# Performance work log

Hardware: AMD Instinct MI355X
Metric: run time of the kernel (lower is better)

Reference implementation:

```python
import jax, jax.numpy as jnp
import numpy as np

HID = 32      # STGAT hidden_dim
HEADS = 8
NHID = HID // HEADS  # per-head hidden = 4
NEG_SLOPE = 0.2


def lstm_layer(x, Wih, Whh, bih, bhh):
    # x: (BN, T, H_in); torch gate order i, f, g, o
    BN = x.shape[0]
    H = Whh.shape[1]
    b = bih + bhh

    def step(carry, xt):
        h, c = carry
        z = xt @ Wih.T + h @ Whh.T + b
        i, f, g, o = jnp.split(z, 4, axis=-1)
        c = jax.nn.sigmoid(f) * c + jax.nn.sigmoid(i) * jnp.tanh(g)
        h = jax.nn.sigmoid(o) * jnp.tanh(c)
        return (h, c), h

    h0 = jnp.zeros((BN, H), x.dtype)
    _, ys = jax.lax.scan(step, (h0, h0), jnp.swapaxes(x, 0, 1))
    return jnp.swapaxes(ys, 0, 1)  # (BN, T, H)


def setup_inputs():
    key = jax.random.key(0)
    ks = jax.random.split(key, 16)
    B, N, T_in, F_in = 8, 300, 12, 3
    T_out, F_out = 12, 3
    X = jax.random.normal(ks[0], (B, N, T_in, F_in), jnp.float32)
    adj = (jax.random.uniform(ks[1], (N, N)) < 0.05).astype(jnp.float32)
    A_hat = jnp.maximum(adj, jnp.eye(N, dtype=jnp.float32))  # self-loops

    def init(k, shape, fan):
        return jax.random.normal(k, shape, jnp.float32) / np.float32(np.sqrt(fan))

    W_gat = init(ks[2], (HID, F_in), F_in)          # linear (no bias)
    a_attn = init(ks[3], (2 * NHID,), 2 * NHID)     # attn (no bias), flattened (1, 2*nhid)
    W_ih0 = init(ks[4], (4 * HID, HID), HID)
    W_hh0 = init(ks[5], (4 * HID, HID), HID)
    b_ih0 = init(ks[6], (4 * HID,), HID)
    b_hh0 = init(ks[7], (4 * HID,), HID)
    W_ih1 = init(ks[8], (4 * HID, HID), HID)
    W_hh1 = init(ks[9], (4 * HID, HID), HID)
    b_ih1 = init(ks[10], (4 * HID,), HID)
    b_hh1 = init(ks[11], (4 * HID,), HID)
    fc_W = init(ks[12], (F_out * T_out, HID), HID)
    fc_b = init(ks[13], (F_out * T_out,), HID)
    return {"A_hat": A_hat, "X": X, "W_gat": W_gat, "a_attn": a_attn,
            "W_ih0": W_ih0, "W_hh0": W_hh0, "b_ih0": b_ih0, "b_hh0": b_hh0,
            "W_ih1": W_ih1, "W_hh1": W_hh1, "b_ih1": b_ih1, "b_hh1": b_hh1,
            "fc_W": fc_W, "fc_b": fc_b}


def reference(A_hat, X, W_gat, a_attn, W_ih0, W_hh0, b_ih0, b_hh0,
              W_ih1, W_hh1, b_ih1, b_hh1, fc_W, fc_b):
    B, N, T, F = X.shape
    T_out = fc_W.shape[0] // F  # nums_feature_output == F here

    # --- GAT, vectorized over (batch, timestep) ---
    # g: (B, N, T, HEADS, NHID)
    g = (X @ W_gat.T).reshape(B, N, T, HEADS, NHID)
    a_l, a_r = a_attn[:NHID], a_attn[NHID:]
    # attn(g_concat) = a_l . g_i + a_r . g_j  (exact split of the concat+linear)
    gl = jnp.einsum('bithd,d->bith', g, a_l)
    gr = jnp.einsum('bjthd,d->bjth', g, a_r)
    e = jax.nn.leaky_relu(gl[:, :, None] + gr[:, None, :], NEG_SLOPE)  # (B,i,j,T,H)
    mask = (A_hat == 0)[None, :, :, None, None]
    e = jnp.where(mask, -jnp.inf, e)
    a = jax.nn.softmax(e, axis=2)  # softmax over j (dim=1 of the (i,j,h) tensor)
    h_gat = jnp.einsum('bijth,bjthd->bithd', a, g).reshape(B, N, T, HID)

    # --- 2-layer LSTM over time, per (b, n) sequence ---
    lstm_in = h_gat.reshape(B * N, T, HID)
    h1 = lstm_layer(lstm_in, W_ih0, W_hh0, b_ih0, b_hh0)
    h2 = lstm_layer(h1, W_ih1, W_hh1, b_ih1, b_hh1)
    h_last = h2[:, -1, :]  # (B*N, HID)

    out = h_last @ fc_W.T + fc_b
    return out.reshape(B, N, T_out, F)
```

## Files before the change

### kernel.cpp

```cpp
#include <hip/hip_runtime.h>

typedef __attribute__((ext_vector_type(8))) short s8v;
typedef __attribute__((ext_vector_type(4))) float f4v;

__device__ __forceinline__ float sgm(float x) { return 1.f / (1.f + __expf(-x)); }
__device__ __forceinline__ float tanh_fast(float x) {
    float e = __expf(-2.f * fabsf(x));
    float t = (1.f - e) / (1.f + e);
    return copysignf(t, x);
}
__device__ __forceinline__ void bsplit(float x, short& hi, short& lo) {
    unsigned u = __float_as_uint(x);
    unsigned hb = u & 0xffff0000u;
    hi = (short)(hb >> 16);
    float r = x - __uint_as_float(hb);
    lo = (short)(__float_as_uint(r) >> 16);
}

#define SQ 10

__device__ __forceinline__ void zcomp(const short* vh, const short* vl,
    const s8v (&ah)[2], const s8v (&al)[2], f4v bias, float* zdst,
    int boff, int g, int w, int n16)
{
    s8v bh0 = *(const s8v*)((const char*)vh + boff +      g*16);
    s8v bh1 = *(const s8v*)((const char*)vh + boff + 64 + g*16);
    s8v bl0 = *(const s8v*)((const char*)vl + boff +      g*16);
    s8v bl1 = *(const s8v*)((const char*)vl + boff + 64 + g*16);
    f4v acc = bias;
    acc = __builtin_amdgcn_mfma_f32_16x16x32_bf16(ah[0], bh0, acc, 0, 0, 0);
    acc = __builtin_amdgcn_mfma_f32_16x16x32_bf16(ah[1], bh1, acc, 0, 0, 0);
    acc = __builtin_amdgcn_mfma_f32_16x16x32_bf16(al[0], bh0, acc, 0, 0, 0);
    acc = __builtin_amdgcn_mfma_f32_16x16x32_bf16(al[1], bh1, acc, 0, 0, 0);
    acc = __builtin_amdgcn_mfma_f32_16x16x32_bf16(ah[0], bl0, acc, 0, 0, 0);
    acc = __builtin_amdgcn_mfma_f32_16x16x32_bf16(ah[1], bl1, acc, 0, 0, 0);
    *(f4v*)&zdst[n16*132 + w*16 + g*4] = acc;
}

__device__ __forceinline__ float cellupd(const float* zbp, int us, int uc, float& cst)
{
    float zi = zbp[us*132 + uc],      zf = zbp[us*132 + 32 + uc];
    float zg = zbp[us*132 + 64 + uc], zo = zbp[us*132 + 96 + uc];
    cst = sgm(zf)*cst + sgm(zi)*tanh_fast(zg);
    return sgm(zo)*tanh_fast(cst);
}

__global__ __launch_bounds__(512, 1) void k_stgat(
    const float* __restrict__ A,    const float* __restrict__ X,
    const float* __restrict__ Wg,   const float* __restrict__ aat,
    const float* __restrict__ Wih0, const float* __restrict__ Whh0,
    const float* __restrict__ bih0, const float* __restrict__ bhh0,
    const float* __restrict__ Wih1, const float* __restrict__ Whh1,
    const float* __restrict__ bih1, const float* __restrict__ bhh1,
    const float* __restrict__ fcW,  const float* __restrict__ fcb,
    float* __restrict__ out)
{
    __shared__ int   snbr[SQ][64];
    __shared__ int   scnt[SQ];
    __shared__ float shg[SQ*384];
    __shared__ __align__(16) short vh0[16*72], vl0[16*72];
    __shared__ __align__(16) short vh1[16*72], vl1[16*72];
    __shared__ __align__(16) float zb0[16*132], zb1[16*132];
    __shared__ float sh1f[SQ*32];

    const int tid  = threadIdx.x;
    const int w    = tid >> 6;
    const int l    = tid & 63;
    const int seq0 = blockIdx.x * SQ;

    for (int r = w; r < SQ; r += 8) {
        int i = (seq0 + r) % 300;
        int c = 0;
        for (int j0 = 0; j0 < 300; j0 += 64) {
            int j = j0 + l;
            bool p = (j < 300) && (A[i*300 + j] != 0.f);
            unsigned long long m = __ballot(p);
            if (p) {
                int pos = __popcll(m & ((1ull << l) - 1ull));
                if (c + pos < 64) snbr[r][c + pos] = j;
            }
            c += __popcll(m);
        }
        if (c > 64) c = 64;
        if (l == 0) scnt[r] = c;
    }

    const int n16  = l & 15;
    const int g    = l >> 4;
    const int zrow = w*16 + n16;
    s8v a0h[2], a0l[2], a1h[2], a1l[2];
    {
        const float* s00 = Wih0 + zrow*32 + g*8;
        const float* s01 = Whh0 + zrow*32 + g*8;
        const float* s10 = Wih1 + zrow*32 + g*8;
        const float* s11 = Whh1 + zrow*32 + g*8;
        #pragma unroll
        for (int j = 0; j < 8; j++) {
            short hh, ll;
            bsplit(s00[j], hh, ll); a0h[0][j]=hh; a0l[0][j]=ll;
            bsplit(s01[j], hh, ll); a0h[1][j]=hh; a0l[1][j]=ll;
            bsplit(s10[j], hh, ll); a1h[0][j]=hh; a1l[0][j]=ll;
            bsplit(s11[j], hh, ll); a1h[1][j]=hh; a1l[1][j]=ll;
        }
    }
    f4v bias0, bias1;
    #pragma unroll
    for (int r = 0; r < 4; r++) {
        int rr = w*16 + g*4 + r;
        bias0[r] = bih0[rr] + bhh0[rr];
        bias1[r] = bih1[rr] + bhh1[rr];
    }

    __syncthreads();

    {
        const int h = l >> 3, j8 = l & 7, d = j8 & 3;
        float wal0=0.f, wal1=0.f, wal2=0.f, war0=0.f, war1=0.f, war2=0.f;
        #pragma unroll
        for (int dd = 0; dd < 4; dd++) {
            float av = aat[dd], bv = aat[4+dd];
            const float* wr = Wg + (h*4+dd)*3;
            wal0 += wr[0]*av; wal1 += wr[1]*av; wal2 += wr[2]*av;
            war0 += wr[0]*bv; war1 += wr[1]*bv; war2 += wr[2]*bv;
        }
        const float* wp = Wg + (h*4+d)*3;
        float wp0 = wp[0], wp1 = wp[1], wp2 = wp[2];

        for (int q = 0; q < 15; q++) {
            int u  = w*15 + q;
            int us = u / 12, t = u - us*12;
            int seq = seq0 + us;
            int b = seq / 300, i = seq - b*300;
            int c = scnt[us];

            const float* Xb = X + (size_t)b*300*36 + t*3;
            const float* Xi = Xb + i*36;
            float gl = Xi[0]*wal0 + Xi[1]*wal1 + Xi[2]*wal2;

            float m = -1e30f, s = 0.f, a0 = 0.f, a1 = 0.f, a2 = 0.f;
            for (int kk = j8; kk < c; kk += 8) {
                int j = snbr[us][kk];
                const float* Xj = Xb + j*36;
                float y0 = Xj[0], y1 = Xj[1], y2 = Xj[2];
                float e = gl + y0*war0 + y1*war1 + y2*war2;
                e = e > 0.f ? e : 0.2f*e;
                if (e > m) {
                    float sc = __expf(m - e);
                    s = s*sc + 1.f;
                    a0 = a0*sc + y0; a1 = a1*sc + y1; a2 = a2*sc + y2;
                    m = e;
                } else {
                    float wt = __expf(e - m);
                    s += wt;
                    a0 += wt*y0; a1 += wt*y1; a2 += wt*y2;
                }
            }
            #pragma unroll
            for (int off = 1; off <= 4; off <<= 1) {
                float m2 = __shfl_xor(m, off, 64);
                float s2 = __shfl_xor(s, off, 64);
                float b0 = __shfl_xor(a0, off, 64);
                float b1 = __shfl_xor(a1, off, 64);
                float b2 = __shfl_xor(a2, off, 64);
                float mo = fmaxf(m, m2);
                float w1 = __expf(m - mo), w2 = __expf(m2 - mo);
                s = s*w1 + s2*w2;
                a0 = a0*w1 + b0*w2; a1 = a1*w1 + b1*w2; a2 = a2*w1 + b2*w2;
                m = mo;
            }
            if (j8 < 4)
                shg[us*384 + t*32 + h*4 + d] = (a0*wp0 + a1*wp1 + a2*wp2) / s;
        }
    }
    __syncthreads();

    const int us = tid >> 5, uc = tid & 31;
    const bool upd = tid < SQ*32;
    const int boff = n16 * 144;

    if (upd) {
        short hh, ll;
        bsplit(shg[us*384 + uc], hh, ll);
        vh0[us*72 + uc] = hh;      vl0[us*72 + uc] = ll;
        vh0[us*72 + 32 + uc] = 0;  vl0[us*72 + 32 + uc] = 0;
        vh1[us*72 + uc] = 0;       vl1[us*72 + uc] = 0;
        vh1[us*72 + 32 + uc] = 0;  vl1[us*72 + 32 + uc] = 0;
    }
    __syncthreads();

    float c0 = 0.f, c1 = 0.f;

    zcomp(vh0, vl0, a0h, a0l, bias0, zb0, boff, g, w, n16);
    __syncthreads();
    if (upd) {
        float h0v = cellupd(zb0, us, uc, c0);
        short hh, ll; bsplit(h0v, hh, ll);
        vh0[us*72 + 32 + uc] = hh;  vl0[us*72 + 32 + uc] = ll;
        vh1[us*72 + uc]      = hh;  vl1[us*72 + uc]      = ll;
        bsplit(shg[us*384 + 32 + uc], hh, ll);
        vh0[us*72 + uc] = hh;  vl0[us*72 + uc] = ll;
    }
    __syncthreads();

    for (int t = 0; t < 12; t++) {
        zcomp(vh1, vl1, a1h, a1l, bias1, zb1, boff, g, w, n16);
        if (t < 11)
            zcomp(vh0, vl0, a0h, a0l, bias0, zb0, boff, g, w, n16);
        __syncthreads();
        if (upd) {
            float h1v = cellupd(zb1, us, uc, c1);
            short hh, ll; bsplit(h1v, hh, ll);
            vh1[us*72 + 32 + uc] = hh;  vl1[us*72 + 32 + uc] = ll;
            if (t == 11) sh1f[us*32 + uc] = h1v;
            if (t < 11) {
                float h0v = cellupd(zb0, us, uc, c0);
                bsplit(h0v, hh, ll);
                vh0[us*72 + 32 + uc] = hh;  vl0[us*72 + 32 + uc] = ll;
                vh1[us*72 + uc]      = hh;  vl1[us*72 + uc]      = ll;
                if (t + 2 < 12) {
                    bsplit(shg[us*384 + (t+2)*32 + uc], hh, ll);
                    vh0[us*72 + uc] = hh;  vl0[us*72 + uc] = ll;
                }
            }
        }
        __syncthreads();
    }

    if (tid < SQ*36) {
        int s = tid / 36, r = tid - s*36;
        float acc = fcb[r];
        #pragma unroll
        for (int c4 = 0; c4 < 8; c4++) {
            float4 uv = *(const float4*)&fcW[r*32 + 4*c4];
            acc += uv.x*sh1f[s*32+4*c4+0] + uv.y*sh1f[s*32+4*c4+1]
                 + uv.z*sh1f[s*32+4*c4+2] + uv.w*sh1f[s*32+4*c4+3];
        }
        out[(seq0 + s)*36 + r] = acc;
    }
}

extern "C" void kernel_launch(void* const* d_in, const int* in_sizes, int n_in,
                              void* d_out, int out_size, void* d_ws, size_t ws_size,
                              hipStream_t stream)
{
    const float* A    = (const float*)d_in[0];
    const float* X    = (const float*)d_in[1];
    const float* Wg   = (const float*)d_in[2];
    const float* aat  = (const float*)d_in[3];
    const float* Wih0 = (const float*)d_in[4];
    const float* Whh0 = (const float*)d_in[5];
    const float* bih0 = (const float*)d_in[6];
    const float* bhh0 = (const float*)d_in[7];
    const float* Wih1 = (const float*)d_in[8];
    const float* Whh1 = (const float*)d_in[9];
    const float* bih1 = (const float*)d_in[10];
    const float* bhh1 = (const float*)d_in[11];
    const float* fcW  = (const float*)d_in[12];
    const float* fcb  = (const float*)d_in[13];
    float* out = (float*)d_out;

    k_stgat<<<240, 512, 0, stream>>>(A, X, Wg, aat,
                                     Wih0, Whh0, bih0, bhh0,
                                     Wih1, Whh1, bih1, bhh1,
                                     fcW, fcb, out);
}
```

Before: 44.00 us.

## Halve sequences per block, stage X in LDS, keep LSTM gates in registers

Each block now handles 5 sequences instead of 10, which doubles the grid to 480 blocks, and launch bounds now allow several blocks per CU. The batch's X slice is copied into shared memory so the GAT neighbour gathers read LDS instead of global memory. The gate rows of the weight matrices are permuted so that each lane's MFMA output holds i, f, g and o for one unit, and the cell update happens in registers without the z buffers in shared memory. The costs are a 43 KB shared area per block, an extra X copy per block, and half of the 16 MFMA columns doing wasted work.

```diff
diff --git a/kernel.cpp b/kernel.cpp
--- a/kernel.cpp
+++ b/kernel.cpp
@@ -17,11 +17,10 @@
     lo = (short)(__float_as_uint(r) >> 16);
 }
 
-#define SQ 10
-
-__device__ __forceinline__ void zcomp(const short* vh, const short* vl,
-    const s8v (&ah)[2], const s8v (&al)[2], f4v bias, float* zdst,
-    int boff, int g, int w, int n16)
+#define SQ 5
+
+__device__ __forceinline__ f4v zA(const short* vh, const short* vl,
+    const s8v (&ah)[2], const s8v (&al)[2], f4v bias, int boff, int g)
 {
     s8v bh0 = *(const s8v*)((const char*)vh + boff +      g*16);
     s8v bh1 = *(const s8v*)((const char*)vh + boff + 64 + g*16);
@@ -34,18 +33,10 @@
     acc = __builtin_amdgcn_mfma_f32_16x16x32_bf16(al[1], bh1, acc, 0, 0, 0);
     acc = __builtin_amdgcn_mfma_f32_16x16x32_bf16(ah[0], bl0, acc, 0, 0, 0);
     acc = __builtin_amdgcn_mfma_f32_16x16x32_bf16(ah[1], bl1, acc, 0, 0, 0);
-    *(f4v*)&zdst[n16*132 + w*16 + g*4] = acc;
-}
-
-__device__ __forceinline__ float cellupd(const float* zbp, int us, int uc, float& cst)
-{
-    float zi = zbp[us*132 + uc],      zf = zbp[us*132 + 32 + uc];
-    float zg = zbp[us*132 + 64 + uc], zo = zbp[us*132 + 96 + uc];
-    cst = sgm(zf)*cst + sgm(zi)*tanh_fast(zg);
-    return sgm(zo)*tanh_fast(cst);
-}
-
-__global__ __launch_bounds__(512, 1) void k_stgat(
+    return acc;
+}
+
+__global__ __launch_bounds__(512, 4) void k_stgat(
     const float* __restrict__ A,    const float* __restrict__ X,
     const float* __restrict__ Wg,   const float* __restrict__ aat,
     const float* __restrict__ Wih0, const float* __restrict__ Whh0,
@@ -58,18 +49,21 @@
     __shared__ int   snbr[SQ][64];
     __shared__ int   scnt[SQ];
     __shared__ float shg[SQ*384];
-    __shared__ __align__(16) short vh0[16*72], vl0[16*72];
-    __shared__ __align__(16) short vh1[16*72], vl1[16*72];
-    __shared__ __align__(16) float zb0[16*132], zb1[16*132];
-    __shared__ float sh1f[SQ*32];
-
+    __shared__ __align__(16) char uarea[43200];
     const int tid  = threadIdx.x;
     const int w    = tid >> 6;
     const int l    = tid & 63;
     const int seq0 = blockIdx.x * SQ;
-
-    for (int r = w; r < SQ; r += 8) {
-        int i = (seq0 + r) % 300;
+    const int b    = seq0 / 300, i0 = seq0 - b*300;
+
+    float* Xs = (float*)uarea;
+
+    {
+        const float* Xg = X + (size_t)b * 10800;
+        for (int x = tid; x < 10800; x += 512) Xs[x] = Xg[x];
+    }
+    if (w < SQ) {
+        int i = i0 + w;
         int c = 0;
         for (int j0 = 0; j0 < 300; j0 += 64) {
             int j = j0 + l;
@@ -77,23 +71,24 @@
             unsigned long long m = __ballot(p);
             if (p) {
                 int pos = __popcll(m & ((1ull << l) - 1ull));
-                if (c + pos < 64) snbr[r][c + pos] = j;
+                if (c + pos < 64) snbr[w][c + pos] = j;
             }
             c += __popcll(m);
         }
         if (c > 64) c = 64;
-        if (l == 0) scnt[r] = c;
-    }
-
-    const int n16  = l & 15;
-    const int g    = l >> 4;
-    const int zrow = w*16 + n16;
+        if (l == 0) scnt[w] = c;
+    }
+
+    const int n16 = l & 15;
+    const int g   = l >> 4;
+    const int cc  = w*4 + g;
+    const int arow = (n16 & 3)*32 + w*4 + (n16 >> 2);
     s8v a0h[2], a0l[2], a1h[2], a1l[2];
     {
-        const float* s00 = Wih0 + zrow*32 + g*8;
-        const float* s01 = Whh0 + zrow*32 + g*8;
-        const float* s10 = Wih1 + zrow*32 + g*8;
-        const float* s11 = Whh1 + zrow*32 + g*8;
+        const float* s00 = Wih0 + arow*32 + g*8;
+        const float* s01 = Whh0 + arow*32 + g*8;
+        const float* s10 = Wih1 + arow*32 + g*8;
+        const float* s11 = Whh1 + arow*32 + g*8;
         #pragma unroll
         for (int j = 0; j < 8; j++) {
             short hh, ll;
@@ -106,9 +101,9 @@
     f4v bias0, bias1;
     #pragma unroll
     for (int r = 0; r < 4; r++) {
-        int rr = w*16 + g*4 + r;
-        bias0[r] = bih0[rr] + bhh0[rr];
-        bias1[r] = bih1[rr] + bhh1[rr];
+        int br = r*32 + cc;
+        bias0[r] = bih0[br] + bhh0[br];
+        bias1[r] = bih1[br] + bhh1[br];
     }
 
     __syncthreads();
@@ -126,21 +121,18 @@
         const float* wp = Wg + (h*4+d)*3;
         float wp0 = wp[0], wp1 = wp[1], wp2 = wp[2];
 
-        for (int q = 0; q < 15; q++) {
-            int u  = w*15 + q;
+        for (int u = w; u < SQ*12; u += 8) {
             int us = u / 12, t = u - us*12;
-            int seq = seq0 + us;
-            int b = seq / 300, i = seq - b*300;
+            int i = i0 + us;
             int c = scnt[us];
 
-            const float* Xb = X + (size_t)b*300*36 + t*3;
-            const float* Xi = Xb + i*36;
+            const float* Xi = Xs + i*36 + t*3;
             float gl = Xi[0]*wal0 + Xi[1]*wal1 + Xi[2]*wal2;
 
             float m = -1e30f, s = 0.f, a0 = 0.f, a1 = 0.f, a2 = 0.f;
             for (int kk = j8; kk < c; kk += 8) {
                 int j = snbr[us][kk];
-                const float* Xj = Xb + j*36;
+                const float* Xj = Xs + j*36 + t*3;
                 float y0 = Xj[0], y1 = Xj[1], y2 = Xj[2];
                 float e = gl + y0*war0 + y1*war1 + y2*war2;
                 e = e > 0.f ? e : 0.2f*e;
@@ -174,53 +166,64 @@
     }
     __syncthreads();
 
-    const int us = tid >> 5, uc = tid & 31;
-    const bool upd = tid < SQ*32;
+    short* vh0 = (short*)uarea;
+    short* vl0 = vh0 + 16*72;
+    short* vh1 = vl0 + 16*72;
+    short* vl1 = vh1 + 16*72;
+    float* sh1f = (float*)(vl1 + 16*72);
+
+    for (int x = tid; x < 16*72; x += 512) {
+        vh0[x] = 0; vl0[x] = 0; vh1[x] = 0; vl1[x] = 0;
+    }
+    __syncthreads();
+    if (tid < SQ*32) {
+        int us = tid >> 5, uc = tid & 31;
+        short hh, ll; bsplit(shg[us*384 + uc], hh, ll);
+        vh0[us*72 + uc] = hh;  vl0[us*72 + uc] = ll;
+    }
+    __syncthreads();
+
     const int boff = n16 * 144;
-
-    if (upd) {
-        short hh, ll;
-        bsplit(shg[us*384 + uc], hh, ll);
-        vh0[us*72 + uc] = hh;      vl0[us*72 + uc] = ll;
-        vh0[us*72 + 32 + uc] = 0;  vl0[us*72 + 32 + uc] = 0;
-        vh1[us*72 + uc] = 0;       vl1[us*72 + uc] = 0;
-        vh1[us*72 + 32 + uc] = 0;  vl1[us*72 + 32 + uc] = 0;
-    }
-    __syncthreads();
-
     float c0 = 0.f, c1 = 0.f;
 
-    zcomp(vh0, vl0, a0h, a0l, bias0, zb0, boff, g, w, n16);
-    __syncthreads();
-    if (upd) {
-        float h0v = cellupd(zb0, us, uc, c0);
+    {
+        f4v z = zA(vh0, vl0, a0h, a0l, bias0, boff, g);
+        __syncthreads();
+        c0 = sgm(z[1])*c0 + sgm(z[0])*tanh_fast(z[2]);
+        float h0v = sgm(z[3])*tanh_fast(c0);
         short hh, ll; bsplit(h0v, hh, ll);
-        vh0[us*72 + 32 + uc] = hh;  vl0[us*72 + 32 + uc] = ll;
-        vh1[us*72 + uc]      = hh;  vl1[us*72 + uc]      = ll;
-        bsplit(shg[us*384 + 32 + uc], hh, ll);
-        vh0[us*72 + uc] = hh;  vl0[us*72 + uc] = ll;
-    }
-    __syncthreads();
+        vh0[n16*72 + 32 + cc] = hh;  vl0[n16*72 + 32 + cc] = ll;
+        vh1[n16*72 + cc]      = hh;  vl1[n16*72 + cc]      = ll;
+        if (tid < SQ*32) {
+            int us = tid >> 5, uc = tid & 31;
+            bsplit(shg[us*384 + 32 + uc], hh, ll);
+            vh0[us*72 + uc] = hh;  vl0[us*72 + uc] = ll;
+        }
+        __syncthreads();
+    }
 
     for (int t = 0; t < 12; t++) {
-        zcomp(vh1, vl1, a1h, a1l, bias1, zb1, boff, g, w, n16);
+        f4v z1 = zA(vh1, vl1, a1h, a1l, bias1, boff, g);
+        f4v z0;
         if (t < 11)
-            zcomp(vh0, vl0, a0h, a0l, bias0, zb0, boff, g, w, n16);
-        __syncthreads();
-        if (upd) {
-            float h1v = cellupd(zb1, us, uc, c1);
-            short hh, ll; bsplit(h1v, hh, ll);
-            vh1[us*72 + 32 + uc] = hh;  vl1[us*72 + 32 + uc] = ll;
-            if (t == 11) sh1f[us*32 + uc] = h1v;
-            if (t < 11) {
-                float h0v = cellupd(zb0, us, uc, c0);
-                bsplit(h0v, hh, ll);
-                vh0[us*72 + 32 + uc] = hh;  vl0[us*72 + 32 + uc] = ll;
-                vh1[us*72 + uc]      = hh;  vl1[us*72 + uc]      = ll;
-                if (t + 2 < 12) {
-                    bsplit(shg[us*384 + (t+2)*32 + uc], hh, ll);
-                    vh0[us*72 + uc] = hh;  vl0[us*72 + uc] = ll;
-                }
+            z0 = zA(vh0, vl0, a0h, a0l, bias0, boff, g);
+        __syncthreads();
+        c1 = sgm(z1[1])*c1 + sgm(z1[0])*tanh_fast(z1[2]);
+        float h1v = sgm(z1[3])*tanh_fast(c1);
+        short hh, ll; bsplit(h1v, hh, ll);
+        vh1[n16*72 + 32 + cc] = hh;  vl1[n16*72 + 32 + cc] = ll;
+        if (t == 11) {
+            if (n16 < SQ) sh1f[n16*32 + cc] = h1v;
+        } else {
+            c0 = sgm(z0[1])*c0 + sgm(z0[0])*tanh_fast(z0[2]);
+            float h0v = sgm(z0[3])*tanh_fast(c0);
+            bsplit(h0v, hh, ll);
+            vh0[n16*72 + 32 + cc] = hh;  vl0[n16*72 + 32 + cc] = ll;
+            vh1[n16*72 + cc]      = hh;  vl1[n16*72 + cc]      = ll;
+            if (tid < SQ*32 && t + 2 < 12) {
+                int us = tid >> 5, uc = tid & 31;
+                short h2, l2; bsplit(shg[us*384 + (t+2)*32 + uc], h2, l2);
+                vh0[us*72 + uc] = h2;  vl0[us*72 + uc] = l2;
             }
         }
         __syncthreads();
@@ -259,7 +262,7 @@
     const float* fcb  = (const float*)d_in[13];
     float* out = (float*)d_out;
 
-    k_stgat<<<240, 512, 0, stream>>>(A, X, Wg, aat,
+    k_stgat<<<480, 512, 0, stream>>>(A, X, Wg, aat,
                                      Wih0, Whh0, bih0, bhh0,
                                      Wih1, Whh1, bih1, bhh1,
                                      fcW, fcb, out);
```

After: 44.10 us. About the same (+0.2%).
